# Kernel optimization log

Measured on AMD Instinct MI355X. Metric: run time of the kernel, lower is better.

Reference implementation:

```python
import jax, jax.numpy as jnp
import numpy as np

D_MODEL = 1024
NUM_HEADS = 16
SEG = 512            # segment_size
DIL = 4              # dilation_rate
HEAD_DIM = D_MODEL // NUM_HEADS


def setup_inputs() -> dict:
    key = jax.random.key(0)
    ks = jax.random.split(key, 5)
    B, S = 4, 4096
    sc = D_MODEL ** -0.5  # keep projected activations O(1) so softmax is not saturated
    def w(k):
        return jax.random.normal(k, (D_MODEL, D_MODEL), jnp.float32) * sc
    z = jnp.zeros((D_MODEL,), jnp.float32)
    return {
        "x": jax.random.normal(ks[0], (B, S, D_MODEL), jnp.float32),
        "Wq": w(ks[1]), "bq": z,
        "Wk": w(ks[2]), "bk": z,
        "Wv": w(ks[3]), "bv": z,
        "Wo": w(ks[4]), "bo": z,
    }


def reference(x, Wq, bq, Wk, bk, Wv, bv, Wo, bo):
    B, S, D = x.shape
    H, hd, seg, r = NUM_HEADS, HEAD_DIM, SEG, DIL
    scaling = hd ** -0.5

    Q = x @ Wq + bq
    K = x @ Wk + bk
    V = x @ Wv + bv

    pad = (-S) % seg
    if pad:
        Q = jnp.pad(Q, ((0, 0), (0, pad), (0, 0)))
        K = jnp.pad(K, ((0, 0), (0, pad), (0, 0)))
        V = jnp.pad(V, ((0, 0), (0, pad), (0, 0)))
    n = (S + pad) // seg          # num_segments
    sd = seg // r                 # dilated positions per segment per head

    # [B, n, sd, r, H, hd]: position within segment = t*r + offset
    def split(t):
        return t.reshape(B, n, sd, r, H, hd)

    offs = jnp.arange(H) % r      # per-head dilation offset sj = j % r
    hidx = jnp.arange(H)
    # vectorized per-head dilated gather -> [B, n, sd, H, hd]
    Qs = split(Q)[:, :, :, offs, hidx, :]
    Ks = split(K)[:, :, :, offs, hidx, :]
    Vs = split(V)[:, :, :, offs, hidx, :]

    # diagonal q.k score per dilated position, softmax over the segment's dilated positions
    scores = jnp.einsum('bnshd,bnshd->bnsh', Qs, Ks) * scaling
    probs = jax.nn.softmax(scores, axis=2)
    attn = probs[..., None] * Vs  # [B, n, sd, H, hd]

    # scatter back to each head's dilated positions; other positions stay zero
    out = jnp.zeros((B, n, sd, r, H, hd), x.dtype)
    out = out.at[:, :, :, offs, hidx, :].set(attn)
    out = out.reshape(B, n * seg, D)[:, :S]
    return out @ Wo + bo
```

## Files before the change

### kernel.cpp

```cpp
#include <hip/hip_runtime.h>
#include <hip/hip_bf16.h>

typedef unsigned short u16;
typedef unsigned int u32;
typedef __attribute__((ext_vector_type(8))) __bf16 bf16x8;
typedef __attribute__((ext_vector_type(4))) float f32x4;

#define NB 4
#define SQ 4096
#define DM 1024
#define RPC 4096
#define S4 (4 * DM)

#define VMCNT(n) asm volatile("s_waitcnt vmcnt(" #n ")" ::: "memory")
#define BARRIER() asm volatile("s_barrier" ::: "memory")

__device__ __forceinline__ u16 f2b(float f) {
  u32 u = __builtin_bit_cast(u32, f);
  u32 r = u + 0x7fffu + ((u >> 16) & 1u);
  return (u16)(r >> 16);
}
__device__ __forceinline__ u32 cvt2(float lo, float hi) {
  u16 a = __builtin_bit_cast(u16, __float2bfloat16(lo));
  u16 b = __builtin_bit_cast(u16, __float2bfloat16(hi));
  return (u32)a | ((u32)b << 16);
}
__device__ __forceinline__ float dot2(u32 q, u32 k) {
  float ql = __builtin_bit_cast(float, q << 16);
  float qh = __builtin_bit_cast(float, q & 0xffff0000u);
  float kl = __builtin_bit_cast(float, k << 16);
  float kh = __builtin_bit_cast(float, k & 0xffff0000u);
  return ql * kl + qh * kh;
}
__device__ __forceinline__ u32 mul2(u32 v, float p) {
  float lo = __builtin_bit_cast(float, v << 16) * p;
  float hi = __builtin_bit_cast(float, v & 0xffff0000u) * p;
  return (u32)f2b(lo) | ((u32)f2b(hi) << 16);
}
__device__ __forceinline__ void gll16(const void* g, void* l) {
  __builtin_amdgcn_global_load_lds(
      (const __attribute__((address_space(1))) void*)g,
      (__attribute__((address_space(3))) void*)l, 16, 0, 0);
}

__global__ __launch_bounds__(256) void prep(const float* __restrict__ x,
                                            const float* __restrict__ Wq,
                                            const float* __restrict__ Wk,
                                            const float* __restrict__ Wv,
                                            const float* __restrict__ Wo,
                                            const float* __restrict__ bq,
                                            const float* __restrict__ bk,
                                            const float* __restrict__ bv,
                                            u16* __restrict__ xbT,
                                            u16* __restrict__ WTp,
                                            u16* __restrict__ WoTp,
                                            float* __restrict__ biasp) {
  __shared__ float T[64][65];
  const int bid = blockIdx.x;
  const int tid = threadIdx.x;
  if (bid < 1024) {
    const int wv = tid >> 6, l = tid & 63;
    const int gr0 = bid * 16 + wv * 4;
#pragma unroll
    for (int it = 0; it < 4; ++it) {
      const int gr = gr0 + it;
      const int c = gr >> 12, pr = gr & 4095;
      const int b = pr >> 10;
      const int srow = ((pr & 1023) << 2) + c;
      const int m0 = pr >> 8, rloc = pr & 255;
      const float* src = x + ((size_t)(b * SQ) + srow) * DM;
      u16* dimg = xbT + (size_t)((c * 16 + m0) * 16) * 16384 + rloc * 64;
      const int swzbase = ((((l & 15) >> 1) ^ (rloc & 7)) << 3) + (l & 1) * 4;
#pragma unroll
      for (int i = 0; i < 4; ++i) {
        float4 v = *reinterpret_cast<const float4*>(src + i * 256 + l * 4);
        uint2 pk;
        pk.x = cvt2(v.x, v.y);
        pk.y = cvt2(v.z, v.w);
        const int k64 = i * 4 + (l >> 4);
        *reinterpret_cast<uint2*>(dimg + (size_t)k64 * 16384 + swzbase) = pk;
      }
    }
  } else if (bid < 1792) {
    const int q = bid - 1024;
    const int c = q / 192;
    const int rem = q - c * 192;
    const int j0 = (rem >> 4) * 64;
    const int k0 = (rem & 15) * 64;
    const int msel = j0 >> 8;
    const float* W = (msel == 0) ? Wq : ((msel == 1) ? Wk : Wv);
    const int slot = (j0 & 255) >> 6;
    const int colbase = (c + 4 * slot) * 64;
    const int rr = tid >> 6, cc = tid & 63;
#pragma unroll
    for (int it = 0; it < 16; ++it) {
      const int kk = rr + it * 4;
      T[kk][cc] = W[(size_t)(k0 + kk) * 1024 + colbase + cc];
    }
    __syncthreads();
    const int k64 = k0 >> 6;
    const int u = cc >> 3, e = cc & 7;
#pragma unroll
    for (int it = 0; it < 16; ++it) {
      const int jj = rr + it * 4;
      const int j = j0 + jj;
      const int n0 = j / 192, nrow = j - n0 * 192;
      WTp[((size_t)((c * 4 + n0) * 16 + k64)) * 12288 + nrow * 64 + (((u ^ (nrow & 7))) << 3) + e] =
          f2b(T[cc][jj]);
    }
  } else if (bid < 2048) {
    const int q = bid - 1792;
    const int c = q >> 6;
    const int rem = q & 63;
    const int e0 = (rem >> 2) * 64;
    const int j0 = (rem & 3) * 64;
    const int rowbase = c * 64 + (j0 >> 6) * 256;
    const int rr = tid >> 6, cc = tid & 63;
#pragma unroll
    for (int it = 0; it < 16; ++it) {
      const int jj = rr + it * 4;
      T[jj][cc] = Wo[(size_t)(rowbase + jj) * 1024 + e0 + cc];
    }
    __syncthreads();
    const int k64 = j0 >> 6;
    const int u = cc >> 3, e = cc & 7;
#pragma unroll
    for (int it = 0; it < 16; ++it) {
      const int ee = rr + it * 4;
      const int n = e0 + ee;
      const int n0 = n >> 8, nrow = n & 255;
      WoTp[((size_t)((c * 4 + n0) * 4 + k64)) * 16384 + nrow * 64 + (((u ^ (nrow & 7))) << 3) + e] =
          f2b(T[cc][ee]);
    }
  } else {
    const int idx = (bid - 2048) * 256 + tid;
    if (idx < 3072) {
      const int c = idx / 768, j = idx % 768;
      const int msel = j >> 8, jj = j & 255;
      const int col = (c + 4 * (jj >> 6)) * 64 + (jj & 63);
      const float* bb = (msel == 0) ? bq : ((msel == 1) ? bk : bv);
      biasp[idx] = bb[col];
    }
  }
}

__global__ __launch_bounds__(256, 2) void gemm_qkv(const u16* __restrict__ xbT,
                                                   const u16* __restrict__ WTp,
                                                   const float* __restrict__ biasp,
                                                   u16* __restrict__ QKV) {
  __shared__ __align__(16) u16 As2[2 * 8192];
  __shared__ __align__(16) u16 Bs2[2 * 12288];
  const int p = blockIdx.x;
  const int L = (p & 7) * 64 + (p >> 3);
  const int c = L >> 7, r = L & 127;
  const int m0 = r >> 2, n0 = r & 3;
  const int tid = threadIdx.x;
  const int lane = tid & 63, w = tid >> 6;
  const int wm = w >> 1, wn = w & 1;
  const int l15 = lane & 15, l16 = lane >> 4;

  const u16* Asrc = xbT + (size_t)((c * 16 + (m0 >> 1)) * 16) * 16384 + (m0 & 1) * 8192;
  const u16* Bsrc = WTp + (size_t)((c * 4 + n0) * 16) * 12288;

  f32x4 acc[4][6];
#pragma unroll
  for (int i = 0; i < 4; ++i)
#pragma unroll
    for (int j = 0; j < 6; ++j) acc[i][j] = (f32x4){0.f, 0.f, 0.f, 0.f};

  int abase[2], bbase[2];
#pragma unroll
  for (int kk = 0; kk < 2; ++kk) {
    const int unit = kk * 4 + l16;
    abase[kk] = (wm * 64 + l15) * 64 + ((unit ^ (l15 & 7)) << 3);
    bbase[kk] = (wn * 96 + l15) * 64 + ((unit ^ (l15 & 7)) << 3);
  }

#define ISSUE_A(kt, buf)                                                   \
  {                                                                        \
    _Pragma("unroll") for (int i = 0; i < 4; ++i)                          \
        gll16(Asrc + (size_t)(kt) * 16384 + i * 2048 + tid * 8,            \
              (char*)As2 + (buf) * 16384 + i * 4096 + tid * 16);           \
  }
#define ISSUE_B(kt, buf)                                                   \
  {                                                                        \
    _Pragma("unroll") for (int i = 0; i < 6; ++i)                          \
        gll16(Bsrc + (size_t)(kt) * 12288 + i * 2048 + tid * 8,            \
              (char*)Bs2 + (buf) * 24576 + i * 4096 + tid * 16);           \
  }

  ISSUE_A(0, 0);
  ISSUE_B(0, 0);
  ISSUE_A(1, 1);
  ISSUE_B(1, 1);
  VMCNT(10);
  BARRIER();

#pragma unroll 1
  for (int t = 0; t < 16; ++t) {
    const u16* Ab = As2 + (t & 1) * 8192;
    const u16* Bb = Bs2 + (t & 1) * 12288;
#pragma unroll
    for (int kk = 0; kk < 2; ++kk) {
      bf16x8 af[4], bv[6];
#pragma unroll
      for (int mf = 0; mf < 4; ++mf)
        af[mf] = *reinterpret_cast<const bf16x8*>(Ab + abase[kk] + mf * 1024);
#pragma unroll
      for (int nf = 0; nf < 6; ++nf)
        bv[nf] = *reinterpret_cast<const bf16x8*>(Bb + bbase[kk] + nf * 1024);
      __builtin_amdgcn_s_setprio(1);
#pragma unroll
      for (int mf = 0; mf < 4; ++mf)
#pragma unroll
        for (int nf = 0; nf < 6; ++nf)
          acc[mf][nf] = __builtin_amdgcn_mfma_f32_16x16x32_bf16(af[mf], bv[nf], acc[mf][nf], 0, 0, 0);
      __builtin_amdgcn_s_setprio(0);
    }
    if (t == 15) break;
    BARRIER();
    if (t <= 13) {
      ISSUE_A(t + 2, t & 1);
      ISSUE_B(t + 2, t & 1);
      VMCNT(10);
    } else {
      VMCNT(0);
    }
    BARRIER();
  }
#undef ISSUE_A
#undef ISSUE_B

  const int rbase = m0 * 128;
  u16* outc = QKV + (size_t)c * RPC * 768;
#pragma unroll
  for (int mf = 0; mf < 4; ++mf) {
#pragma unroll
    for (int nf = 0; nf < 6; ++nf) {
      const int gcol = n0 * 192 + wn * 96 + nf * 16 + l15;
      const float bias = biasp[c * 768 + gcol];
#pragma unroll
      for (int jj = 0; jj < 4; ++jj) {
        const int rowt = wm * 64 + mf * 16 + l16 * 4 + jj;
        outc[(size_t)(rbase + rowt) * 768 + gcol] = f2b(acc[mf][nf][jj] + bias);
      }
    }
  }
}

__global__ __launch_bounds__(256) void attn_k(const u16* __restrict__ QKV,
                                              u16* __restrict__ attnYp) {
  __shared__ float sc[4][128];
  const int blk = blockIdx.x;
  const int c = blk >> 6, b = (blk >> 4) & 3, n = (blk >> 1) & 7, half = blk & 1;
  const int r0 = b * 1024 + n * 128;
  const int m0 = r0 >> 8;
  const int rb = r0 & 255;
  const u16* base = QKV + ((size_t)c * RPC + r0) * 768;
  const int tid = threadIdx.x;
#pragma unroll
  for (int it = 0; it < 2; ++it) {
    const int tt = tid + it * 256;
    const int t = tt & 127, slot = tt >> 7;
    const u16* q = base + (size_t)t * 768 + slot * 64;
    float s = 0.f;
#pragma unroll
    for (int dd = 0; dd < 8; ++dd) {
      uint4 qa = *reinterpret_cast<const uint4*>(q + dd * 8);
      uint4 ka = *reinterpret_cast<const uint4*>(q + 256 + dd * 8);
      s += dot2(qa.x, ka.x) + dot2(qa.y, ka.y) + dot2(qa.z, ka.z) + dot2(qa.w, ka.w);
    }
    sc[slot][t] = s * 0.125f;
  }
  __syncthreads();
  const int w = tid >> 6, lane = tid & 63;
  float v0 = sc[w][lane], v1 = sc[w][lane + 64];
  float m = fmaxf(v0, v1);
#pragma unroll
  for (int off = 32; off; off >>= 1) m = fmaxf(m, __shfl_xor(m, off));
  float e0 = __expf(v0 - m), e1 = __expf(v1 - m);
  float ssum = e0 + e1;
#pragma unroll
  for (int off = 32; off; off >>= 1) ssum += __shfl_xor(ssum, off);
  const float inv = 1.f / ssum;
  sc[w][lane] = e0 * inv;
  sc[w][lane + 64] = e1 * inv;
  __syncthreads();
  u16* yout = attnYp + (size_t)((c * 16 + m0) * 4) * 16384;
#pragma unroll
  for (int it = 0; it < 8; ++it) {
    const int vi = tid + it * 256;
    const int t = vi >> 4, c8 = (vi & 15) + half * 16;
    const float pr = sc[c8 >> 3][t];
    uint4 va = *reinterpret_cast<const uint4*>(base + (size_t)t * 768 + 512 + c8 * 8);
    uint4 ra;
    ra.x = mul2(va.x, pr); ra.y = mul2(va.y, pr); ra.z = mul2(va.z, pr); ra.w = mul2(va.w, pr);
    const int rloc = rb + t;
    const int k64 = c8 >> 3, uu = c8 & 7, pp = uu ^ (rloc & 7);
    *reinterpret_cast<uint4*>(yout + k64 * 16384 + rloc * 64 + pp * 8) = ra;
  }
}

__global__ __launch_bounds__(512, 1) void gemm_out(const u16* __restrict__ attnYp,
                                                   const u16* __restrict__ WoTp,
                                                   const float* __restrict__ bo,
                                                   float* __restrict__ out) {
  __shared__ __align__(16) u16 As[2][16384];
  __shared__ __align__(16) u16 Bs[2][16384];
  const int p = blockIdx.x;
  const int L = (p & 7) * 32 + (p >> 3);
  const int c = L >> 6, rem = L & 63;
  const int m0 = rem >> 2, n0 = rem & 3;
  const int tid = threadIdx.x;
  const int lane = tid & 63, w = tid >> 6;
  const int wm = w >> 1, wn = w & 1;
  const int l15 = lane & 15, l16 = lane >> 4;

  const u16* Asrc = attnYp + (size_t)((c * 16 + m0) * 4) * 16384;
  const u16* Bsrc = WoTp + (size_t)((c * 4 + n0) * 4) * 16384;

  f32x4 acc[4][8];
#pragma unroll
  for (int i = 0; i < 4; ++i)
#pragma unroll
    for (int j = 0; j < 8; ++j) acc[i][j] = (f32x4){0.f, 0.f, 0.f, 0.f};

  int aoff[2][4], boff[2][8];
#pragma unroll
  for (int kk = 0; kk < 2; ++kk) {
    const int unit = kk * 4 + l16;
#pragma unroll
    for (int mf = 0; mf < 4; ++mf) {
      const int r = wm * 64 + mf * 16 + l15;
      aoff[kk][mf] = r * 64 + ((unit ^ (r & 7)) << 3);
    }
#pragma unroll
    for (int nf = 0; nf < 8; ++nf) {
      const int r = wn * 128 + nf * 16 + l15;
      boff[kk][nf] = r * 64 + ((unit ^ (r & 7)) << 3);
    }
  }

#define ISSUE(kt, buf)                                                     \
  {                                                                        \
    _Pragma("unroll") for (int i = 0; i < 4; ++i) {                        \
      gll16(Asrc + (size_t)(kt) * 16384 + tid * 8 + i * 4096,              \
            (char*)&As[buf][0] + tid * 16 + i * 8192);                     \
      gll16(Bsrc + (size_t)(kt) * 16384 + tid * 8 + i * 4096,              \
            (char*)&Bs[buf][0] + tid * 16 + i * 8192);                     \
    }                                                                      \
  }

  ISSUE(0, 0);
  ISSUE(1, 1);
  VMCNT(8);
  BARRIER();

#pragma unroll 1
  for (int t = 0; t < 4; ++t) {
    const u16* Ab = As[t & 1];
    const u16* Bb = Bs[t & 1];
#pragma unroll
    for (int kk = 0; kk < 2; ++kk) {
      bf16x8 af[4], bv[8];
#pragma unroll
      for (int mf = 0; mf < 4; ++mf) af[mf] = *reinterpret_cast<const bf16x8*>(Ab + aoff[kk][mf]);
#pragma unroll
      for (int nf = 0; nf < 8; ++nf) bv[nf] = *reinterpret_cast<const bf16x8*>(Bb + boff[kk][nf]);
      __builtin_amdgcn_s_setprio(1);
#pragma unroll
      for (int mf = 0; mf < 4; ++mf)
#pragma unroll
        for (int nf = 0; nf < 8; ++nf)
          acc[mf][nf] = __builtin_amdgcn_mfma_f32_16x16x32_bf16(af[mf], bv[nf], acc[mf][nf], 0, 0, 0);
      __builtin_amdgcn_s_setprio(0);
    }
    if (t == 3) break;
    BARRIER();
    if (t <= 1) {
      ISSUE(t + 2, t & 1);
      VMCNT(8);
    } else {
      VMCNT(0);
    }
    BARRIER();
  }
#undef ISSUE

  const int rbase = m0 * 256;
  const int b = rbase >> 10;
  const int sbase = ((rbase & 1023) << 2) + c;
  float* outp = out + (size_t)(b * SQ + sbase) * DM;
#pragma unroll
  for (int mf = 0; mf < 4; ++mf) {
#pragma unroll
    for (int nf = 0; nf < 8; ++nf) {
      const int gcol = n0 * 256 + wn * 128 + nf * 16 + l15;
      const float bias = bo[gcol];
#pragma unroll
      for (int jj = 0; jj < 4; ++jj) {
        const int rowt = wm * 64 + mf * 16 + l16 * 4 + jj;
        outp[(size_t)rowt * S4 + gcol] = acc[mf][nf][jj] + bias;
      }
    }
  }
}

extern "C" void kernel_launch(void* const* d_in, const int* in_sizes, int n_in,
                              void* d_out, int out_size, void* d_ws, size_t ws_size,
                              hipStream_t stream) {
  const float* x  = (const float*)d_in[0];
  const float* Wq = (const float*)d_in[1];
  const float* bq = (const float*)d_in[2];
  const float* Wk = (const float*)d_in[3];
  const float* bk = (const float*)d_in[4];
  const float* Wv = (const float*)d_in[5];
  const float* bv = (const float*)d_in[6];
  const float* Wo = (const float*)d_in[7];
  const float* bo = (const float*)d_in[8];
  float* out = (float*)d_out;

  char* ws = (char*)d_ws;
  u16* xbT    = (u16*)(ws);
  u16* WoTp   = (u16*)(ws + 33554432);
  u16* attnYp = (u16*)(ws + 35651584);

  char* ob = (char*)d_out;
  u16*   QKV   = (u16*)(ob);
  u16*   WTp   = (u16*)(ob + 33554432);
  float* biasp = (float*)(ob + 39845888);

  prep<<<2060, 256, 0, stream>>>(x, Wq, Wk, Wv, Wo, bq, bk, bv, xbT, WTp, WoTp, biasp);
  gemm_qkv<<<512, 256, 0, stream>>>(xbT, WTp, biasp, QKV);
  attn_k<<<256, 256, 0, stream>>>(QKV, attnYp);
  gemm_out<<<256, 512, 0, stream>>>(attnYp, WoTp, bo, out);
}
```

Before: 88.33 us.

## Fuse dilated attention softmax into output projection GEMM prologue

Removes the separate attention kernel and its attnY intermediate buffer. The output GEMM now computes q·k scores and the softmax for its own 256-row tile, then scales V rows by the probabilities in registers and writes them straight into the swizzled LDS A tiles, pipelined alongside the Wo global-to-LDS loads. This saves one launch and a global write/read round trip of the attention output. In exchange the GEMM gets a serial score/softmax prologue, and each of the four column blocks (n0) redundantly recomputes the same scores. QKV moves into the workspace, since the output buffer is now written while QKV is still being read.

```diff
diff --git a/kernel.cpp b/kernel.cpp
--- a/kernel.cpp
+++ b/kernel.cpp
@@ -13,6 +13,7 @@
 #define S4 (4 * DM)
 
 #define VMCNT(n) asm volatile("s_waitcnt vmcnt(" #n ")" ::: "memory")
+#define LGKM0()  asm volatile("s_waitcnt lgkmcnt(0)" ::: "memory")
 #define BARRIER() asm volatile("s_barrier" ::: "memory")
 
 __device__ __forceinline__ u16 f2b(float f) {
@@ -248,65 +249,13 @@
   }
 }
 
-__global__ __launch_bounds__(256) void attn_k(const u16* __restrict__ QKV,
-                                              u16* __restrict__ attnYp) {
-  __shared__ float sc[4][128];
-  const int blk = blockIdx.x;
-  const int c = blk >> 6, b = (blk >> 4) & 3, n = (blk >> 1) & 7, half = blk & 1;
-  const int r0 = b * 1024 + n * 128;
-  const int m0 = r0 >> 8;
-  const int rb = r0 & 255;
-  const u16* base = QKV + ((size_t)c * RPC + r0) * 768;
-  const int tid = threadIdx.x;
-#pragma unroll
-  for (int it = 0; it < 2; ++it) {
-    const int tt = tid + it * 256;
-    const int t = tt & 127, slot = tt >> 7;
-    const u16* q = base + (size_t)t * 768 + slot * 64;
-    float s = 0.f;
-#pragma unroll
-    for (int dd = 0; dd < 8; ++dd) {
-      uint4 qa = *reinterpret_cast<const uint4*>(q + dd * 8);
-      uint4 ka = *reinterpret_cast<const uint4*>(q + 256 + dd * 8);
-      s += dot2(qa.x, ka.x) + dot2(qa.y, ka.y) + dot2(qa.z, ka.z) + dot2(qa.w, ka.w);
-    }
-    sc[slot][t] = s * 0.125f;
-  }
-  __syncthreads();
-  const int w = tid >> 6, lane = tid & 63;
-  float v0 = sc[w][lane], v1 = sc[w][lane + 64];
-  float m = fmaxf(v0, v1);
-#pragma unroll
-  for (int off = 32; off; off >>= 1) m = fmaxf(m, __shfl_xor(m, off));
-  float e0 = __expf(v0 - m), e1 = __expf(v1 - m);
-  float ssum = e0 + e1;
-#pragma unroll
-  for (int off = 32; off; off >>= 1) ssum += __shfl_xor(ssum, off);
-  const float inv = 1.f / ssum;
-  sc[w][lane] = e0 * inv;
-  sc[w][lane + 64] = e1 * inv;
-  __syncthreads();
-  u16* yout = attnYp + (size_t)((c * 16 + m0) * 4) * 16384;
-#pragma unroll
-  for (int it = 0; it < 8; ++it) {
-    const int vi = tid + it * 256;
-    const int t = vi >> 4, c8 = (vi & 15) + half * 16;
-    const float pr = sc[c8 >> 3][t];
-    uint4 va = *reinterpret_cast<const uint4*>(base + (size_t)t * 768 + 512 + c8 * 8);
-    uint4 ra;
-    ra.x = mul2(va.x, pr); ra.y = mul2(va.y, pr); ra.z = mul2(va.z, pr); ra.w = mul2(va.w, pr);
-    const int rloc = rb + t;
-    const int k64 = c8 >> 3, uu = c8 & 7, pp = uu ^ (rloc & 7);
-    *reinterpret_cast<uint4*>(yout + k64 * 16384 + rloc * 64 + pp * 8) = ra;
-  }
-}
-
-__global__ __launch_bounds__(512, 1) void gemm_out(const u16* __restrict__ attnYp,
+__global__ __launch_bounds__(512, 1) void attn_out(const u16* __restrict__ QKV,
                                                    const u16* __restrict__ WoTp,
                                                    const float* __restrict__ bo,
                                                    float* __restrict__ out) {
-  __shared__ __align__(16) u16 As[2][16384];
-  __shared__ __align__(16) u16 Bs[2][16384];
+  __shared__ __align__(16) u16 As2[2 * 16384];
+  __shared__ __align__(16) u16 Bs2[2 * 16384];
+  __shared__ float pL[1024];
   const int p = blockIdx.x;
   const int L = (p & 7) * 32 + (p >> 3);
   const int c = L >> 6, rem = L & 63;
@@ -316,8 +265,85 @@
   const int wm = w >> 1, wn = w & 1;
   const int l15 = lane & 15, l16 = lane >> 4;
 
-  const u16* Asrc = attnYp + (size_t)((c * 16 + m0) * 4) * 16384;
+  const u16* qkv = QKV + ((size_t)c * RPC + m0 * 256) * 768;
   const u16* Bsrc = WoTp + (size_t)((c * 4 + n0) * 4) * 16384;
+
+#pragma unroll
+  for (int it = 0; it < 2; ++it) {
+    const int idx = tid + it * 512;
+    const int row = idx & 255, slot = idx >> 8;
+    const u16* qp = qkv + (size_t)row * 768 + slot * 64;
+    float s = 0.f;
+#pragma unroll
+    for (int dd = 0; dd < 8; ++dd) {
+      uint4 qa = *reinterpret_cast<const uint4*>(qp + dd * 8);
+      uint4 ka = *reinterpret_cast<const uint4*>(qp + 256 + dd * 8);
+      s += dot2(qa.x, ka.x) + dot2(qa.y, ka.y) + dot2(qa.z, ka.z) + dot2(qa.w, ka.w);
+    }
+    pL[slot * 256 + row] = s * 0.125f;
+  }
+  __syncthreads();
+
+  const int vrow = tid >> 1;
+  const int vq = (tid & 1) * 32;
+  const u16* vsrc = qkv + (size_t)vrow * 768 + 512 + vq;
+  uint4 vv0, vv1, vv2, vv3;
+#define LOADV(kt)                                                          \
+  {                                                                        \
+    vv0 = *reinterpret_cast<const uint4*>(vsrc + (kt) * 64);               \
+    vv1 = *reinterpret_cast<const uint4*>(vsrc + (kt) * 64 + 8);           \
+    vv2 = *reinterpret_cast<const uint4*>(vsrc + (kt) * 64 + 16);          \
+    vv3 = *reinterpret_cast<const uint4*>(vsrc + (kt) * 64 + 24);          \
+  }
+#define ISSUE_BO(kt, buf)                                                  \
+  {                                                                        \
+    _Pragma("unroll") for (int i = 0; i < 4; ++i)                          \
+        gll16(Bsrc + (size_t)(kt) * 16384 + i * 4096 + tid * 8,            \
+              (char*)Bs2 + (buf) * 32768 + i * 8192 + tid * 16);           \
+  }
+  const int aw0 = vrow * 64 + ((((tid & 1) * 4) ^ (vrow & 7)) << 3);
+  const int aw1 = vrow * 64 + (((((tid & 1) * 4) + 1) ^ (vrow & 7)) << 3);
+  const int aw2 = vrow * 64 + (((((tid & 1) * 4) + 2) ^ (vrow & 7)) << 3);
+  const int aw3 = vrow * 64 + (((((tid & 1) * 4) + 3) ^ (vrow & 7)) << 3);
+#define WRITEA(kt, buf)                                                    \
+  {                                                                        \
+    const float pr = pL[(kt) * 256 + vrow];                                \
+    u16* ab = As2 + (buf) * 16384;                                         \
+    uint4 r0, r1, r2, r3;                                                  \
+    r0.x = mul2(vv0.x, pr); r0.y = mul2(vv0.y, pr);                        \
+    r0.z = mul2(vv0.z, pr); r0.w = mul2(vv0.w, pr);                        \
+    r1.x = mul2(vv1.x, pr); r1.y = mul2(vv1.y, pr);                        \
+    r1.z = mul2(vv1.z, pr); r1.w = mul2(vv1.w, pr);                        \
+    r2.x = mul2(vv2.x, pr); r2.y = mul2(vv2.y, pr);                        \
+    r2.z = mul2(vv2.z, pr); r2.w = mul2(vv2.w, pr);                        \
+    r3.x = mul2(vv3.x, pr); r3.y = mul2(vv3.y, pr);                        \
+    r3.z = mul2(vv3.z, pr); r3.w = mul2(vv3.w, pr);                        \
+    *reinterpret_cast<uint4*>(ab + aw0) = r0;                              \
+    *reinterpret_cast<uint4*>(ab + aw1) = r1;                              \
+    *reinterpret_cast<uint4*>(ab + aw2) = r2;                              \
+    *reinterpret_cast<uint4*>(ab + aw3) = r3;                              \
+  }
+
+  LOADV(0);
+  ISSUE_BO(0, 0);
+  ISSUE_BO(1, 1);
+
+  {
+    const int slot = w >> 1, seg = w & 1;
+    float* sv = &pL[slot * 256 + seg * 128];
+    const float v0 = sv[lane], v1 = sv[lane + 64];
+    float m = fmaxf(v0, v1);
+#pragma unroll
+    for (int off = 32; off; off >>= 1) m = fmaxf(m, __shfl_xor(m, off));
+    const float e0 = __expf(v0 - m), e1 = __expf(v1 - m);
+    float ssum = e0 + e1;
+#pragma unroll
+    for (int off = 32; off; off >>= 1) ssum += __shfl_xor(ssum, off);
+    const float inv = 1.f / ssum;
+    sv[lane] = e0 * inv;
+    sv[lane + 64] = e1 * inv;
+  }
+  __syncthreads();
 
   f32x4 acc[4][8];
 #pragma unroll
@@ -331,61 +357,58 @@
     const int unit = kk * 4 + l16;
 #pragma unroll
     for (int mf = 0; mf < 4; ++mf) {
-      const int r = wm * 64 + mf * 16 + l15;
-      aoff[kk][mf] = r * 64 + ((unit ^ (r & 7)) << 3);
+      const int rr = wm * 64 + mf * 16 + l15;
+      aoff[kk][mf] = rr * 64 + ((unit ^ (rr & 7)) << 3);
     }
 #pragma unroll
     for (int nf = 0; nf < 8; ++nf) {
-      const int r = wn * 128 + nf * 16 + l15;
-      boff[kk][nf] = r * 64 + ((unit ^ (r & 7)) << 3);
-    }
-  }
-
-#define ISSUE(kt, buf)                                                     \
-  {                                                                        \
-    _Pragma("unroll") for (int i = 0; i < 4; ++i) {                        \
-      gll16(Asrc + (size_t)(kt) * 16384 + tid * 8 + i * 4096,              \
-            (char*)&As[buf][0] + tid * 16 + i * 8192);                     \
-      gll16(Bsrc + (size_t)(kt) * 16384 + tid * 8 + i * 4096,              \
-            (char*)&Bs[buf][0] + tid * 16 + i * 8192);                     \
-    }                                                                      \
-  }
-
-  ISSUE(0, 0);
-  ISSUE(1, 1);
+      const int rr = wn * 128 + nf * 16 + l15;
+      boff[kk][nf] = rr * 64 + ((unit ^ (rr & 7)) << 3);
+    }
+  }
+
   VMCNT(8);
+  WRITEA(0, 0);
+  LOADV(1);
+  VMCNT(8);
+  LGKM0();
   BARRIER();
 
 #pragma unroll 1
   for (int t = 0; t < 4; ++t) {
-    const u16* Ab = As[t & 1];
-    const u16* Bb = Bs[t & 1];
+    const u16* Ab = As2 + (t & 1) * 16384;
+    const u16* Bb = Bs2 + (t & 1) * 16384;
 #pragma unroll
     for (int kk = 0; kk < 2; ++kk) {
-      bf16x8 af[4], bv[8];
+      bf16x8 af[4], bvv[8];
 #pragma unroll
       for (int mf = 0; mf < 4; ++mf) af[mf] = *reinterpret_cast<const bf16x8*>(Ab + aoff[kk][mf]);
 #pragma unroll
-      for (int nf = 0; nf < 8; ++nf) bv[nf] = *reinterpret_cast<const bf16x8*>(Bb + boff[kk][nf]);
+      for (int nf = 0; nf < 8; ++nf) bvv[nf] = *reinterpret_cast<const bf16x8*>(Bb + boff[kk][nf]);
       __builtin_amdgcn_s_setprio(1);
 #pragma unroll
       for (int mf = 0; mf < 4; ++mf)
 #pragma unroll
         for (int nf = 0; nf < 8; ++nf)
-          acc[mf][nf] = __builtin_amdgcn_mfma_f32_16x16x32_bf16(af[mf], bv[nf], acc[mf][nf], 0, 0, 0);
+          acc[mf][nf] = __builtin_amdgcn_mfma_f32_16x16x32_bf16(af[mf], bvv[nf], acc[mf][nf], 0, 0, 0);
       __builtin_amdgcn_s_setprio(0);
     }
     if (t == 3) break;
     BARRIER();
     if (t <= 1) {
-      ISSUE(t + 2, t & 1);
-      VMCNT(8);
+      ISSUE_BO(t + 2, t & 1);
+      VMCNT(4);
     } else {
       VMCNT(0);
     }
+    WRITEA(t + 1, (t + 1) & 1);
+    if (t <= 1) LOADV(t + 2);
+    LGKM0();
     BARRIER();
   }
-#undef ISSUE
+#undef LOADV
+#undef ISSUE_BO
+#undef WRITEA
 
   const int rbase = m0 * 256;
   const int b = rbase >> 10;
@@ -421,17 +444,15 @@
   float* out = (float*)d_out;
 
   char* ws = (char*)d_ws;
-  u16* xbT    = (u16*)(ws);
-  u16* WoTp   = (u16*)(ws + 33554432);
-  u16* attnYp = (u16*)(ws + 35651584);
+  u16* xbT  = (u16*)(ws);
+  u16* WoTp = (u16*)(ws + 33554432);
+  u16* QKV  = (u16*)(ws + 35651584);
 
   char* ob = (char*)d_out;
-  u16*   QKV   = (u16*)(ob);
   u16*   WTp   = (u16*)(ob + 33554432);
   float* biasp = (float*)(ob + 39845888);
 
   prep<<<2060, 256, 0, stream>>>(x, Wq, Wk, Wv, Wo, bq, bk, bv, xbT, WTp, WoTp, biasp);
   gemm_qkv<<<512, 256, 0, stream>>>(xbT, WTp, biasp, QKV);
-  attn_k<<<256, 256, 0, stream>>>(QKV, attnYp);
-  gemm_out<<<256, 512, 0, stream>>>(attnYp, WoTp, bo, out);
-}
+  attn_out<<<256, 512, 0, stream>>>(QKV, WoTp, bo, out);
+}
```

Result: no change. 88.52 us (+0.2%).
